# Performance work log

Measured on AMD Instinct MI355X. Metric: run time of the kernel, lower is better.

## Reference

```python
import jax, jax.numpy as jnp
import numpy as np

B, N, C, H = 2, 2048, 1024, 16
D = C // H  # head_dim = 64
ROPE_THETA = 500000.0
INIT_STD = 0.02


def setup_inputs() -> dict:
    key = jax.random.key(0)
    ks = jax.random.split(key, 6)
    hidden_states = jax.random.normal(ks[0], (B, N, C), dtype=jnp.float32)
    # rotary embeddings: standard llama-style, built from rope_theta
    inv_freq = jnp.asarray(1.0 / (ROPE_THETA ** (np.arange(0, D, 2, dtype=np.float32) / D)), jnp.float32)
    freqs = jnp.outer(jnp.arange(N, dtype=jnp.float32), inv_freq)  # (N, D/2)
    emb = jnp.concatenate([freqs, freqs], axis=-1)  # (N, D)
    cos = jnp.broadcast_to(jnp.cos(emb)[None], (B, N, D))
    sin = jnp.broadcast_to(jnp.sin(emb)[None], (B, N, D))
    Wq = jax.random.normal(ks[1], (C, C), jnp.float32) * INIT_STD
    Wk = jax.random.normal(ks[2], (C, C), jnp.float32) * INIT_STD
    Wv = jax.random.normal(ks[3], (C, C), jnp.float32) * INIT_STD
    Wo = jax.random.normal(ks[4], (C, C), jnp.float32) * INIT_STD
    return {"hidden_states": hidden_states, "cos": cos, "sin": sin,
            "Wq": Wq, "Wk": Wk, "Wv": Wv, "Wo": Wo}


def _rotate_half(x):
    x1, x2 = x[..., : D // 2], x[..., D // 2 :]
    return jnp.concatenate((-x2, x1), axis=-1)


def reference(hidden_states, cos, sin, Wq, Wk, Wv, Wo):
    scaling = D ** -0.5
    # projections; W stored as (in, out) so y = x @ W
    q = (hidden_states @ Wq) * scaling
    k = hidden_states @ Wk
    v = hidden_states @ Wv
    q = q.reshape(B, N, H, D)
    k = k.reshape(B, N, H, D)
    v = v.reshape(B, N, H, D)
    # RoPE, cos/sin broadcast over heads: (B,N,1,D)
    c = cos[:, :, None, :]
    s = sin[:, :, None, :]
    q = q * c + _rotate_half(q) * s
    k = k * c + _rotate_half(k) * s
    # causal SDPA (q already scaled)
    scores = jnp.einsum("bqhd,bkhd->bhqk", q, k)  # (B,H,N,N)
    causal = jnp.tril(jnp.ones((N, N), dtype=bool))
    scores = jnp.where(causal[None, None], scores, jnp.finfo(scores.dtype).min)
    probs = jax.nn.softmax(scores, axis=-1)
    out = jnp.einsum("bhqk,bkhd->bqhd", probs, v).reshape(B, N, C)
    return out @ Wo
```

## Files before the change

kernel.cpp:

```cpp
#include <hip/hip_runtime.h>
#include <hip/hip_bf16.h>

typedef __hip_bfloat16 bf16;
typedef __attribute__((ext_vector_type(8))) short short8;
typedef __attribute__((ext_vector_type(4))) short short4v;
typedef __attribute__((ext_vector_type(4))) float f32x4;

#define BB 2
#define NN 2048
#define CC 1024
#define HH 16
#define DD 64
#define MM (BB*NN)
#define QKVN 3072
#define LOG2E 1.44269504088896340736f

__device__ __forceinline__ void glds16(const void* g, void* l) {
    __builtin_amdgcn_global_load_lds((const __attribute__((address_space(1))) void*)g,
                                     (__attribute__((address_space(3))) void*)l, 16, 0, 0);
}
__device__ __forceinline__ short pkbf(float x) { bf16 t = (bf16)x; return *(short*)&t; }

__global__ __launch_bounds__(256) void convert_f32_bf16(const float* __restrict__ in,
                                                        bf16* __restrict__ out) {
    int i = blockIdx.x * 256 + threadIdx.x;
    float4 v = ((const float4*)in)[i];
    short4v s;
    s.x = pkbf(v.x); s.y = pkbf(v.y); s.z = pkbf(v.z); s.w = pkbf(v.w);
    *((short4v*)out + i) = s;
}

__global__ __launch_bounds__(256) void transpose4(const float* __restrict__ W0,
                                                  const float* __restrict__ W1,
                                                  const float* __restrict__ W2,
                                                  const float* __restrict__ W3,
                                                  bf16* __restrict__ Wtqkv,
                                                  bf16* __restrict__ Wto) {
    __shared__ float t[32][33];
    const int z = blockIdx.z;
    const float* W = z == 0 ? W0 : (z == 1 ? W1 : (z == 2 ? W2 : W3));
    bf16* dst = z < 3 ? Wtqkv + (size_t)z * CC * CC : Wto;
    const int tx = threadIdx.x, ty = threadIdx.y;
    const int x0 = blockIdx.x * 32, y0 = blockIdx.y * 32;
    #pragma unroll
    for (int i = 0; i < 4; ++i)
        t[ty + i * 8][tx] = W[(size_t)(y0 + ty + i * 8) * CC + x0 + tx];
    __syncthreads();
    #pragma unroll
    for (int i = 0; i < 4; ++i)
        dst[(size_t)(x0 + ty + i * 8) * CC + y0 + tx] = (bf16)t[tx][ty + i * 8];
}

template<int Nn, int MODE>
__global__ __launch_bounds__(256) void gemm2(const bf16* __restrict__ A,
                                             const bf16* __restrict__ Bt,
                                             void* __restrict__ Cout,
                                             const float* __restrict__ cosp,
                                             const float* __restrict__ sinp,
                                             bf16* __restrict__ VtOut) {
    __shared__ __align__(16) bf16 As[128 * 32];
    __shared__ __align__(16) bf16 Bs[128 * 32];
    const int tid = threadIdx.x, lane = tid & 63, wid = tid >> 6;
    const int wr = wid >> 1, wc = wid & 1, l16 = lane & 15, lg = lane >> 4;
    constexpr int GX = Nn / 128;
    constexpr int GY = MM / 128;
    constexpr int CPX = GX * GY / 8;
    const int flat = blockIdx.y * GX + blockIdx.x;
    const int v = (flat & 7) * CPX + (flat >> 3);
    const int n0 = (v % GX) * 128, m0 = (v / GX) * 128;

    f32x4 acc[4][4];
    #pragma unroll
    for (int i = 0; i < 4; ++i)
        #pragma unroll
        for (int j = 0; j < 4; ++j) acc[i][j] = {0.f, 0.f, 0.f, 0.f};

    for (int k0 = 0; k0 < 1024; k0 += 32) {
        #pragma unroll
        for (int ii = 0; ii < 2; ++ii) {
            const int issue = wid * 2 + ii;
            const int a = issue * 1024 + lane * 16;
            const int r = a >> 6, cb = a & 63;
            glds16(&A [(size_t)(m0 + r) * 1024 + k0 + (cb >> 1)], (char*)As + issue * 1024);
            glds16(&Bt[(size_t)(n0 + r) * 1024 + k0 + (cb >> 1)], (char*)Bs + issue * 1024);
        }
        __syncthreads();
        short8 af[4], bfr[4];
        #pragma unroll
        for (int i = 0; i < 4; ++i) af[i]  = *(const short8*)((char*)As + (wr * 64 + i * 16 + l16) * 64 + lg * 16);
        #pragma unroll
        for (int j = 0; j < 4; ++j) bfr[j] = *(const short8*)((char*)Bs + (wc * 64 + j * 16 + l16) * 64 + lg * 16);
        #pragma unroll
        for (int i = 0; i < 4; ++i)
            #pragma unroll
            for (int j = 0; j < 4; ++j)
                acc[i][j] = __builtin_amdgcn_mfma_f32_16x16x32_bf16(af[i], bfr[j], acc[i][j], 0, 0, 0);
        __syncthreads();
    }

    if (MODE == 1 && n0 >= 2 * CC) {
        #pragma unroll
        for (int i = 0; i < 4; ++i) {
            const int row0 = m0 + wr * 64 + i * 16 + lg * 4;
            const int bb = row0 >> 11, nn_ = row0 & (NN - 1);
            #pragma unroll
            for (int j = 0; j < 4; ++j) {
                const int col = n0 - 2 * CC + wc * 64 + j * 16 + l16;
                const int hh = col >> 6, d = col & 63;
                short4v s4;
                #pragma unroll
                for (int r = 0; r < 4; ++r) s4[r] = pkbf(acc[i][j][r]);
                *(short4v*)&VtOut[((size_t)(bb * HH + hh) * DD + d) * NN + nn_] = s4;
            }
        }
    } else if (MODE == 1) {
        const float qs = (n0 < CC) ? 0.125f * LOG2E : 1.0f;
        bf16* Cb = (bf16*)Cout;
        #pragma unroll
        for (int i = 0; i < 4; ++i)
            #pragma unroll
            for (int r = 0; r < 4; ++r) {
                const int row = m0 + wr * 64 + i * 16 + lg * 4 + r;
                #pragma unroll
                for (int j = 0; j < 4; ++j) {
                    const int col = n0 + wc * 64 + j * 16 + l16;
                    const int d = col & 63;
                    const float cv = cosp[(size_t)row * DD + d];
                    const float sv = sinp[(size_t)row * DD + d];
                    const float x = acc[i][j][r], y = acc[i][j ^ 2][r];
                    const float ov = (d < 32) ? (x * cv - y * sv) * qs
                                              : (x * cv + y * sv) * qs;
                    Cb[(size_t)row * QKVN + col] = (bf16)ov;
                }
            }
    } else {
        float* Cf = (float*)Cout;
        #pragma unroll
        for (int i = 0; i < 4; ++i)
            #pragma unroll
            for (int r = 0; r < 4; ++r) {
                const int row = m0 + wr * 64 + i * 16 + lg * 4 + r;
                #pragma unroll
                for (int j = 0; j < 4; ++j)
                    Cf[(size_t)row * Nn + n0 + wc * 64 + j * 16 + l16] = acc[i][j][r];
            }
    }
}

__global__ __launch_bounds__(256) void flash_mfma3(const bf16* __restrict__ QKV,
                                                   const bf16* __restrict__ Vt,
                                                   bf16* __restrict__ Ab) {
    __shared__ __align__(16) bf16 Ks[2][4096];
    __shared__ __align__(16) bf16 Vs[2][4096];
    const int tid = threadIdx.x, lane = tid & 63, wid = tid >> 6;
    const int l16 = lane & 15, lg = lane >> 4;
    const int bid = blockIdx.x;
    const int bh = bid & 31;
    const int qt = 31 - (bid >> 5);
    const int h = bh & (HH - 1), b = bh >> 4;
    const int wq0 = qt * 64 + wid * 16;
    const int nkt = qt + 1;

    const bf16* Kbase = QKV + (size_t)b * NN * QKVN + CC + h * DD;
    const bf16* Vbase = Vt + (size_t)(b * HH + h) * DD * NN;

    short8 qf[2];
    #pragma unroll
    for (int ch = 0; ch < 2; ++ch)
        qf[ch] = *(const short8*)&QKV[(size_t)(b * NN + wq0 + l16) * QKVN
                                      + h * DD + ch * 32 + lg * 8];

    f32x4 o[4];
    #pragma unroll
    for (int dn = 0; dn < 4; ++dn) o[dn] = {0.f, 0.f, 0.f, 0.f};
    float mx = -1e30f, ls = 0.f;

    auto stage = [&](int kt, int bufi) {
        const int k0s = kt * 64;
        #pragma unroll
        for (int ii = 0; ii < 2; ++ii) {
            const int issue = wid * 2 + ii;
            const int a = issue * 1024 + lane * 16;
            const int r = a >> 7;
            const int cb = (a & 127) ^ ((r & 7) << 4);
            glds16(Kbase + (size_t)(k0s + r) * QKVN + (cb >> 1), (char*)&Ks[bufi][0] + issue * 1024);
            glds16(Vbase + (size_t)r * NN + k0s + (cb >> 1),     (char*)&Vs[bufi][0] + issue * 1024);
        }
    };

    stage(0, 0);
    __syncthreads();

    for (int kt = 0; kt < nkt; ++kt) {
        const int k0 = kt * 64;
        const int cur = kt & 1;
        if (kt + 1 < nkt) stage(kt + 1, cur ^ 1);

        f32x4 st[4];
        #pragma unroll
        for (int kc = 0; kc < 4; ++kc) st[kc] = {0.f, 0.f, 0.f, 0.f};
        __builtin_amdgcn_s_setprio(1);
        #pragma unroll
        for (int kc = 0; kc < 4; ++kc) {
            const int row = kc * 16 + l16;
            const char* rb = (const char*)&Ks[cur][0] + row * 128;
            const int sw = (row & 7) << 4;
            short8 kf0 = *(const short8*)(rb + ((lg * 16) ^ sw));
            short8 kf1 = *(const short8*)(rb + ((64 + lg * 16) ^ sw));
            st[kc] = __builtin_amdgcn_mfma_f32_16x16x32_bf16(kf0, qf[0], st[kc], 0, 0, 0);
            st[kc] = __builtin_amdgcn_mfma_f32_16x16x32_bf16(kf1, qf[1], st[kc], 0, 0, 0);
        }
        __builtin_amdgcn_s_setprio(0);

        if (kt == qt) {
            #pragma unroll
            for (int kc = 0; kc < 4; ++kc)
                #pragma unroll
                for (int r = 0; r < 4; ++r)
                    if (k0 + kc * 16 + lg * 4 + r > wq0 + l16) st[kc][r] = -1e30f;
        }

        float rm = fmaxf(fmaxf(st[0][0], st[0][1]), fmaxf(st[0][2], st[0][3]));
        #pragma unroll
        for (int kc = 1; kc < 4; ++kc)
            rm = fmaxf(rm, fmaxf(fmaxf(st[kc][0], st[kc][1]), fmaxf(st[kc][2], st[kc][3])));
        rm = fmaxf(rm, __shfl_xor(rm, 16, 64));
        rm = fmaxf(rm, __shfl_xor(rm, 32, 64));
        if (__any(rm > mx + 8.0f)) {
            const float mn = fmaxf(mx, rm);
            const float sc = exp2f(mx - mn);
            ls *= sc;
            #pragma unroll
            for (int dn = 0; dn < 4; ++dn) {
                o[dn][0] *= sc; o[dn][1] *= sc; o[dn][2] *= sc; o[dn][3] *= sc;
            }
            mx = mn;
        }
        float rs = 0.f;
        #pragma unroll
        for (int kc = 0; kc < 4; ++kc)
            #pragma unroll
            for (int r = 0; r < 4; ++r) {
                const float p = exp2f(st[kc][r] - mx);
                st[kc][r] = p; rs += p;
            }
        rs += __shfl_xor(rs, 16, 64);
        rs += __shfl_xor(rs, 32, 64);
        ls += rs;

        __builtin_amdgcn_s_setprio(1);
        #pragma unroll
        for (int kc = 0; kc < 4; ++kc) {
            short4v pf;
            pf[0] = pkbf(st[kc][0]); pf[1] = pkbf(st[kc][1]);
            pf[2] = pkbf(st[kc][2]); pf[3] = pkbf(st[kc][3]);
            #pragma unroll
            for (int dn = 0; dn < 4; ++dn) {
                const int row = dn * 16 + l16;
                short4v vf = *(const short4v*)((const char*)&Vs[cur][0] + row * 128
                                               + ((kc * 32 + lg * 8) ^ ((row & 7) << 4)));
                o[dn] = __builtin_amdgcn_mfma_f32_16x16x16bf16_1k(vf, pf, o[dn], 0, 0, 0);
            }
        }
        __builtin_amdgcn_s_setprio(0);

        __syncthreads();
    }

    const float inv = 1.f / ls;
    const size_t rowb = (size_t)(b * NN + wq0 + l16) * CC + h * DD;
    #pragma unroll
    for (int dn = 0; dn < 4; ++dn) {
        short4v s4;
        s4[0] = pkbf(o[dn][0] * inv); s4[1] = pkbf(o[dn][1] * inv);
        s4[2] = pkbf(o[dn][2] * inv); s4[3] = pkbf(o[dn][3] * inv);
        *(short4v*)&Ab[rowb + dn * 16 + lg * 4] = s4;
    }
}

extern "C" void kernel_launch(void* const* d_in, const int* in_sizes, int n_in,
                              void* d_out, int out_size, void* d_ws, size_t ws_size,
                              hipStream_t stream) {
    const float* hs   = (const float*)d_in[0];
    const float* cosp = (const float*)d_in[1];
    const float* sinp = (const float*)d_in[2];
    const float* Wq   = (const float*)d_in[3];
    const float* Wk   = (const float*)d_in[4];
    const float* Wv   = (const float*)d_in[5];
    const float* Wo   = (const float*)d_in[6];
    float* out = (float*)d_out;

    char* ws = (char*)d_ws;
    bf16* hsb   = (bf16*)(ws);
    bf16* Wtqkv = (bf16*)(ws + (8  << 20));
    bf16* Wto   = (bf16*)(ws + (14 << 20));
    bf16* QKV   = (bf16*)(ws + (16 << 20));
    bf16* Vtb   = (bf16*)(ws + (40 << 20));
    bf16* Abuf  = hsb;

    convert_f32_bf16<<<MM * CC / 1024, 256, 0, stream>>>(hs, hsb);

    transpose4<<<dim3(32, 32, 4), dim3(32, 8), 0, stream>>>(Wq, Wk, Wv, Wo, Wtqkv, Wto);

    gemm2<QKVN, 1><<<dim3(QKVN / 128, MM / 128), 256, 0, stream>>>(
        hsb, Wtqkv, QKV, cosp, sinp, Vtb);

    flash_mfma3<<<1024, 256, 0, stream>>>(QKV, Vtb, Abuf);

    gemm2<CC, 2><<<dim3(CC / 128, MM / 128), 256, 0, stream>>>(
        Abuf, Wto, out, nullptr, nullptr, nullptr);
}
```

Measured before the change: 139.1 us.

## Double-buffer GEMM LDS tiles and simplify RoPE epilogue

Adds a two-stage LDS buffer to the bf16 GEMM so the next K-slice's global-to-LDS loads are issued while MFMAs run on the current slice, dropping one barrier per iteration. It also removes the XCD-aware block-index swizzle in favour of plain row-major tile mapping, and rewrites the RoPE epilogue to compute paired halves together, halving cos/sin loads. The swizzle removal may hurt L2 locality across XCDs, and doubling LDS use can lower occupancy.

```diff
diff --git a/kernel.cpp b/kernel.cpp
--- a/kernel.cpp
+++ b/kernel.cpp
@@ -52,22 +52,17 @@
 }
 
 template<int Nn, int MODE>
-__global__ __launch_bounds__(256) void gemm2(const bf16* __restrict__ A,
+__global__ __launch_bounds__(256) void gemm3(const bf16* __restrict__ A,
                                              const bf16* __restrict__ Bt,
                                              void* __restrict__ Cout,
                                              const float* __restrict__ cosp,
                                              const float* __restrict__ sinp,
                                              bf16* __restrict__ VtOut) {
-    __shared__ __align__(16) bf16 As[128 * 32];
-    __shared__ __align__(16) bf16 Bs[128 * 32];
+    __shared__ __align__(16) bf16 As[2][128 * 32];
+    __shared__ __align__(16) bf16 Bs[2][128 * 32];
     const int tid = threadIdx.x, lane = tid & 63, wid = tid >> 6;
     const int wr = wid >> 1, wc = wid & 1, l16 = lane & 15, lg = lane >> 4;
-    constexpr int GX = Nn / 128;
-    constexpr int GY = MM / 128;
-    constexpr int CPX = GX * GY / 8;
-    const int flat = blockIdx.y * GX + blockIdx.x;
-    const int v = (flat & 7) * CPX + (flat >> 3);
-    const int n0 = (v % GX) * 128, m0 = (v / GX) * 128;
+    const int n0 = blockIdx.x * 128, m0 = blockIdx.y * 128;
 
     f32x4 acc[4][4];
     #pragma unroll
@@ -75,27 +70,34 @@
         #pragma unroll
         for (int j = 0; j < 4; ++j) acc[i][j] = {0.f, 0.f, 0.f, 0.f};
 
-    for (int k0 = 0; k0 < 1024; k0 += 32) {
-        #pragma unroll
-        for (int ii = 0; ii < 2; ++ii) {
-            const int issue = wid * 2 + ii;
-            const int a = issue * 1024 + lane * 16;
-            const int r = a >> 6, cb = a & 63;
-            glds16(&A [(size_t)(m0 + r) * 1024 + k0 + (cb >> 1)], (char*)As + issue * 1024);
-            glds16(&Bt[(size_t)(n0 + r) * 1024 + k0 + (cb >> 1)], (char*)Bs + issue * 1024);
-        }
+    const int issue0 = wid * 2;
+    const int sr0 = (issue0 * 1024 + lane * 16) >> 6;
+    const int sc0 = ((issue0 * 1024 + lane * 16) & 63) >> 1;
+    const int sr1 = ((issue0 + 1) * 1024 + lane * 16) >> 6;
+    const int sc1 = (((issue0 + 1) * 1024 + lane * 16) & 63) >> 1;
+
+    auto stage = [&](int k0, int bufi) {
+        glds16(&A [(size_t)(m0 + sr0) * 1024 + k0 + sc0], (char*)&As[bufi][0] + issue0 * 1024);
+        glds16(&Bt[(size_t)(n0 + sr0) * 1024 + k0 + sc0], (char*)&Bs[bufi][0] + issue0 * 1024);
+        glds16(&A [(size_t)(m0 + sr1) * 1024 + k0 + sc1], (char*)&As[bufi][0] + (issue0 + 1) * 1024);
+        glds16(&Bt[(size_t)(n0 + sr1) * 1024 + k0 + sc1], (char*)&Bs[bufi][0] + (issue0 + 1) * 1024);
+    };
+
+    stage(0, 0);
+    for (int t = 0; t < 32; ++t) {
+        const int cur = t & 1;
         __syncthreads();
+        if (t + 1 < 32) stage((t + 1) * 32, cur ^ 1);
         short8 af[4], bfr[4];
         #pragma unroll
-        for (int i = 0; i < 4; ++i) af[i]  = *(const short8*)((char*)As + (wr * 64 + i * 16 + l16) * 64 + lg * 16);
-        #pragma unroll
-        for (int j = 0; j < 4; ++j) bfr[j] = *(const short8*)((char*)Bs + (wc * 64 + j * 16 + l16) * 64 + lg * 16);
+        for (int i = 0; i < 4; ++i) af[i]  = *(const short8*)((char*)&As[cur][0] + (wr * 64 + i * 16 + l16) * 64 + lg * 16);
+        #pragma unroll
+        for (int j = 0; j < 4; ++j) bfr[j] = *(const short8*)((char*)&Bs[cur][0] + (wc * 64 + j * 16 + l16) * 64 + lg * 16);
         #pragma unroll
         for (int i = 0; i < 4; ++i)
             #pragma unroll
             for (int j = 0; j < 4; ++j)
                 acc[i][j] = __builtin_amdgcn_mfma_f32_16x16x32_bf16(af[i], bfr[j], acc[i][j], 0, 0, 0);
-        __syncthreads();
     }
 
     if (MODE == 1 && n0 >= 2 * CC) {
@@ -122,15 +124,15 @@
             for (int r = 0; r < 4; ++r) {
                 const int row = m0 + wr * 64 + i * 16 + lg * 4 + r;
                 #pragma unroll
-                for (int j = 0; j < 4; ++j) {
-                    const int col = n0 + wc * 64 + j * 16 + l16;
-                    const int d = col & 63;
+                for (int j = 0; j < 2; ++j) {
+                    const int d = j * 16 + l16;
                     const float cv = cosp[(size_t)row * DD + d];
                     const float sv = sinp[(size_t)row * DD + d];
-                    const float x = acc[i][j][r], y = acc[i][j ^ 2][r];
-                    const float ov = (d < 32) ? (x * cv - y * sv) * qs
-                                              : (x * cv + y * sv) * qs;
-                    Cb[(size_t)row * QKVN + col] = (bf16)ov;
+                    const float x1 = acc[i][j][r];
+                    const float x2 = acc[i][j + 2][r];
+                    const size_t cbase = (size_t)row * QKVN + n0 + wc * 64 + j * 16 + l16;
+                    Cb[cbase]      = (bf16)((x1 * cv - x2 * sv) * qs);
+                    Cb[cbase + 32] = (bf16)((x2 * cv + x1 * sv) * qs);
                 }
             }
     } else {
@@ -302,11 +304,11 @@
 
     transpose4<<<dim3(32, 32, 4), dim3(32, 8), 0, stream>>>(Wq, Wk, Wv, Wo, Wtqkv, Wto);
 
-    gemm2<QKVN, 1><<<dim3(QKVN / 128, MM / 128), 256, 0, stream>>>(
+    gemm3<QKVN, 1><<<dim3(QKVN / 128, MM / 128), 256, 0, stream>>>(
         hsb, Wtqkv, QKV, cosp, sinp, Vtb);
 
     flash_mfma3<<<1024, 256, 0, stream>>>(QKV, Vtb, Abuf);
 
-    gemm2<CC, 2><<<dim3(CC / 128, MM / 128), 256, 0, stream>>>(
+    gemm3<CC, 2><<<dim3(CC / 128, MM / 128), 256, 0, stream>>>(
         Abuf, Wto, out, nullptr, nullptr, nullptr);
 }
```

Result: faster. 133.4 us (-4.1%).
